# Performance work log

Hardware: AMD Instinct MI355X
Metric: run time of the kernel (lower is better)

The kernel has to match this reference:

```python
import jax, jax.numpy as jnp
import numpy as np

B, T, D, H, d = 2, 2048, 1024, 16, 64
INNER = H * d
SCALE = d ** -0.5


def _rope(x, inv_freq):
    # x: [B, H, T, d], interleaved rotary as in the torch module
    t = x.shape[2]
    pos = jnp.arange(t, dtype=jnp.float32)
    freqs = pos[:, None] * inv_freq[None, :]          # [T, d/2]
    cos_f, sin_f = jnp.cos(freqs), jnp.sin(freqs)
    x1, x2 = x[..., 0::2], x[..., 1::2]
    y1 = x1 * cos_f - x2 * sin_f
    y2 = x1 * sin_f + x2 * cos_f
    return jnp.stack([y1, y2], axis=-1).reshape(x.shape)


def setup_inputs() -> dict:
    key = jax.random.key(0)
    ks = jax.random.split(key, 6)
    x = jax.random.normal(ks[0], (B, T, D), jnp.float32)
    W_qkv = jax.random.normal(ks[1], (D, 3 * INNER), jnp.float32) * (D ** -0.5)
    W_out = jax.random.normal(ks[2], (INNER, D), jnp.float32) * (INNER ** -0.5)
    W_dt = jax.random.normal(ks[3], (D, H), jnp.float32) * 0.01
    b_dt = jnp.full((H,), -4.0, jnp.float32)
    W_gsp = jax.random.normal(ks[4], (D, INNER), jnp.float32) * 0.01
    b_gsp = jnp.full((INNER,), -3.0, jnp.float32)
    inv_freq = 1.0 / (10000.0 ** (jnp.arange(0, d, 2, dtype=jnp.float32) / d))
    return {"x": x, "W_qkv": W_qkv, "W_out": W_out, "W_dt": W_dt,
            "b_dt": b_dt, "W_gsp": W_gsp, "b_gsp": b_gsp, "inv_freq": inv_freq}


def reference(x, W_qkv, W_out, W_dt, b_dt, W_gsp, b_gsp, inv_freq):
    qkv = (x @ W_qkv).reshape(B, T, 3, H, d)
    Q = jnp.moveaxis(qkv[:, :, 0], 1, 2)   # [B,H,T,d]
    K = jnp.moveaxis(qkv[:, :, 1], 1, 2)
    V = jnp.moveaxis(qkv[:, :, 2], 1, 2)
    Q = _rope(Q, inv_freq)
    K = _rope(K, inv_freq)

    dt = jax.nn.softplus(x @ W_dt + b_dt)             # [B,T,H]
    gamma = jnp.moveaxis(jnp.exp(-dt), 1, 2)          # [B,H,T]

    p = jax.nn.sigmoid(x @ W_gsp + b_gsp).reshape(B, T, H, d)
    p = jnp.moveaxis(p, 1, 2)                          # [B,H,T,d]
    gamma_eff = gamma[..., None] * (1.0 - p) + p
    gamma_scalar = gamma_eff.mean(axis=-1)            # [B,H,T]
    V = V * (1.0 - p)

    log_gamma = jnp.log(jnp.clip(gamma_scalar, 1e-6, 1.0 - 1e-6))
    lgc = jnp.cumsum(log_gamma, axis=-1)              # [B,H,T]
    log_D = jnp.clip(lgc[..., :, None] - lgc[..., None, :], -20.0, 0.0)
    causal = jnp.tril(jnp.ones((T, T), jnp.float32))
    Dm = jnp.exp(log_D) * causal                      # [B,H,T,T]

    Wscore = jnp.einsum('bhtd,bhsd->bhts', Q * SCALE, K)
    A = Wscore * Dm
    Y = jnp.einsum('bhts,bhsd->bhtd', A, V)
    Y = jnp.moveaxis(Y, 1, 2).reshape(B, T, INNER)
    return Y @ W_out
```

## Files before the change

### kernel.cpp

```cpp
#include <hip/hip_runtime.h>
#include <hip/hip_bf16.h>
#include <math.h>

#define B_     2
#define T_     2048
#define D_     1024
#define H_     16
#define INNER_ 1024
#define NC_    4352
#define SCALE_ 0.125f

typedef unsigned short u16;
typedef short short8 __attribute__((ext_vector_type(8)));
typedef float f32x4 __attribute__((ext_vector_type(4)));
typedef unsigned short u16x4 __attribute__((ext_vector_type(4)));

__device__ __forceinline__ u16 f2bf(float x) {
  union { float f; unsigned u; } v; v.f = x;
  unsigned r = v.u + 0x7fffu + ((v.u >> 16) & 1u);
  return (u16)(r >> 16);
}
__device__ __forceinline__ float b2f(u16 x) {
  union { unsigned u; float f; } v; v.u = ((unsigned)x) << 16;
  return v.f;
}
__device__ __forceinline__ void gload16(const void* g, void* l) {
  __builtin_amdgcn_global_load_lds(
      (const __attribute__((address_space(1))) void*)g,
      (__attribute__((address_space(3))) void*)l, 16, 0, 0);
}

__global__ __launch_bounds__(256) void cast_bf16_kernel(
    const float* __restrict__ src, u16* __restrict__ dst, int n4) {
  int i = blockIdx.x * 256 + threadIdx.x;
  if (i >= n4) return;
  float4 v = *reinterpret_cast<const float4*>(src + (size_t)i * 4);
  u16x4 o; o.x = f2bf(v.x); o.y = f2bf(v.y); o.z = f2bf(v.z); o.w = f2bf(v.w);
  *reinterpret_cast<u16x4*>(dst + (size_t)i * 4) = o;
}

__global__ __launch_bounds__(256) void cast_transpose_kernel(
    const float* __restrict__ src, u16* __restrict__ dst, int K, int N) {
  __shared__ float tile[64][65];
  const int k0 = blockIdx.y * 64, n0 = blockIdx.x * 64;
  for (int e = threadIdx.x; e < 4096; e += 256) {
    int kk = e >> 6, nn = e & 63;
    tile[kk][nn] = src[(size_t)(k0 + kk) * N + n0 + nn];
  }
  __syncthreads();
  for (int e = threadIdx.x; e < 4096; e += 256) {
    int nn = e >> 6, kk = e & 63;
    dst[(size_t)(n0 + nn) * K + k0 + kk] = f2bf(tile[kk][nn]);
  }
}

__global__ __launch_bounds__(256) void wdt_transpose_kernel(
    const float* __restrict__ W_dt, u16* __restrict__ dst) {
  int i = blockIdx.x * 256 + threadIdx.x;
  int k = i >> 4, h = i & 15;
  dst[(size_t)h * D_ + k] = f2bf(W_dt[i]);
}

__global__ __launch_bounds__(256) void rope_tab_kernel(
    const float* __restrict__ inv_freq, float2* __restrict__ tab) {
  int i = blockIdx.x * 256 + threadIdx.x;
  int t = i >> 5, j = i & 31;
  float s, c;
  sincosf((float)t * inv_freq[j], &s, &c);
  tab[i] = make_float2(c, s);
}

#define SWZG(r) ((((r) & 3) ^ (((r) >> 2) & 1)))

__device__ __forceinline__ void stage_op(const u16* __restrict__ gbase, int kt,
                                         char* ldst, int h, int tid) {
  int r = h * 128 + (tid >> 2);
  int kg = (tid & 3) ^ SWZG(r);
  gload16(gbase + (size_t)r * D_ + kt * 32 + kg * 8,
          ldst + (h * 128 + (tid >> 6) * 16) * 64);
}
__device__ __forceinline__ short8 ldfrag(const char* tile, int row, int g4) {
  return *(const short8*)(tile + row * 64 + ((g4 ^ SWZG(row)) << 4));
}

__global__ __launch_bounds__(512, 2) void gemm_big(
    const u16* __restrict__ A, const u16* __restrict__ Bt,
    u16* __restrict__ C) {
  __shared__ char lds[4 * 32768];
  const int tid = threadIdx.x;
  const int w = tid >> 6, l = tid & 63;
  const int bid = blockIdx.x;
  const int xcd = bid & 7, j = bid >> 3;
  const int brow = xcd * 2 + (j >= 17 ? 1 : 0);
  const int bcol = (j >= 17) ? j - 17 : j;
  const int m0 = brow * 256, n0 = bcol * 256;
  const int wr = (w >> 2) * 128, wc = (w & 3) * 64;
  const int ql = l & 15, g4 = l >> 4;

  const u16* Ag = A + (size_t)m0 * D_;
  const u16* Bg = Bt + (size_t)n0 * D_;

  f32x4 acc[8][4] = {};

#pragma unroll
  for (int t = 0; t < 3; ++t) {
    char* bufA = lds + t * 32768;
    char* bufB = bufA + 16384;
    stage_op(Ag, t, bufA, 0, tid); stage_op(Ag, t, bufA, 1, tid);
    stage_op(Bg, t, bufB, 0, tid); stage_op(Bg, t, bufB, 1, tid);
  }

  const int NT = D_ / 32;
  for (int kt = 0; kt < NT; ++kt) {
    if (kt < NT - 2)       asm volatile("s_waitcnt vmcnt(8)" ::: "memory");
    else if (kt == NT - 2) asm volatile("s_waitcnt vmcnt(4)" ::: "memory");
    else                   asm volatile("s_waitcnt vmcnt(0)" ::: "memory");
    __builtin_amdgcn_sched_barrier(0);
    __builtin_amdgcn_s_barrier();
    __builtin_amdgcn_sched_barrier(0);

    char* bufA = lds + (kt & 3) * 32768;
    char* bufB = bufA + 16384;
    char* nbufA = lds + ((kt + 3) & 3) * 32768;
    char* nbufB = nbufA + 16384;
    const bool pre = (kt + 3 < NT);

    if (pre) {
      stage_op(Ag, kt + 3, nbufA, 0, tid);
      stage_op(Ag, kt + 3, nbufA, 1, tid);
    }
    short8 bf[4];
#pragma unroll
    for (int nf = 0; nf < 4; ++nf) bf[nf] = ldfrag(bufB, wc + nf * 16 + ql, g4);
    short8 af[4];
#pragma unroll
    for (int mf = 0; mf < 4; ++mf) af[mf] = ldfrag(bufA, wr + mf * 16 + ql, g4);
    __builtin_amdgcn_s_setprio(1);
#pragma unroll
    for (int mf = 0; mf < 4; ++mf)
#pragma unroll
      for (int nf = 0; nf < 4; ++nf)
        acc[mf][nf] = __builtin_amdgcn_mfma_f32_16x16x32_bf16(af[mf], bf[nf], acc[mf][nf], 0, 0, 0);
    __builtin_amdgcn_s_setprio(0);

    if (pre) {
      stage_op(Bg, kt + 3, nbufB, 0, tid);
      stage_op(Bg, kt + 3, nbufB, 1, tid);
    }
    short8 af2[4];
#pragma unroll
    for (int mf = 0; mf < 4; ++mf) af2[mf] = ldfrag(bufA, wr + 64 + mf * 16 + ql, g4);
    __builtin_amdgcn_s_setprio(1);
#pragma unroll
    for (int mf = 0; mf < 4; ++mf)
#pragma unroll
      for (int nf = 0; nf < 4; ++nf)
        acc[mf + 4][nf] = __builtin_amdgcn_mfma_f32_16x16x32_bf16(af2[mf], bf[nf], acc[mf + 4][nf], 0, 0, 0);
    __builtin_amdgcn_s_setprio(0);
  }

#pragma unroll
  for (int mf = 0; mf < 8; ++mf) {
#pragma unroll
    for (int r = 0; r < 4; ++r) {
      size_t row = (size_t)(m0 + wr + mf * 16 + g4 * 4 + r);
      size_t base = row * NC_ + n0 + wc + ql;
#pragma unroll
      for (int nf = 0; nf < 4; ++nf)
        C[base + nf * 16] = f2bf(acc[mf][nf][r]);
    }
  }
}

template <bool BF16OUT>
__global__ __launch_bounds__(256) void gemm_bt(
    const u16* __restrict__ A, const u16* __restrict__ Bt,
    void* __restrict__ Cv, int M, int N, int K) {
  __shared__ u16 As[128 * 64] __attribute__((aligned(16)));
  __shared__ u16 Bs[128 * 64] __attribute__((aligned(16)));
  const int tid = threadIdx.x;
  const int w = tid >> 6, l = tid & 63;
  const int m0 = blockIdx.y * 128, n0 = blockIdx.x * 128;
  const int wr = (w >> 1) * 64, wc = (w & 1) * 64;
  const int srow = l >> 3;
  const int kgrp = ((l & 7) ^ srow) * 8;

  f32x4 acc[4][4] = {};

  for (int kt = 0; kt < K; kt += 64) {
    if (kt) __syncthreads();
#pragma unroll
    for (int i = 0; i < 4; ++i) {
      int c = w * 4 + i;
      int row = c * 8 + srow;
      gload16(A + (size_t)(m0 + row) * K + kt + kgrp, (char*)As + c * 1024);
      gload16(Bt + (size_t)(n0 + row) * K + kt + kgrp, (char*)Bs + c * 1024);
    }
    __syncthreads();
#pragma unroll
    for (int kk = 0; kk < 2; ++kk) {
      short8 af[4], bf[4];
#pragma unroll
      for (int i = 0; i < 4; ++i) {
        int ra = wr + i * 16 + (l & 15);
        int sa = kk * 4 + (l >> 4);
        af[i] = *(const short8*)((const char*)As + ra * 128 + ((sa ^ (ra & 7)) << 4));
        int rb = wc + i * 16 + (l & 15);
        bf[i] = *(const short8*)((const char*)Bs + rb * 128 + ((sa ^ (rb & 7)) << 4));
      }
#pragma unroll
      for (int i = 0; i < 4; ++i)
#pragma unroll
        for (int j = 0; j < 4; ++j)
          acc[i][j] = __builtin_amdgcn_mfma_f32_16x16x32_bf16(af[i], bf[j], acc[i][j], 0, 0, 0);
    }
  }
#pragma unroll
  for (int i = 0; i < 4; ++i) {
#pragma unroll
    for (int r = 0; r < 4; ++r) {
      size_t row = (size_t)(m0 + wr + i * 16 + (l >> 4) * 4 + r);
      size_t base = row * N + n0 + wc + (l & 15);
#pragma unroll
      for (int j = 0; j < 4; ++j) {
        if (BF16OUT) ((u16*)Cv)[base + j * 16] = f2bf(acc[i][j][r]);
        else         ((float*)Cv)[base + j * 16] = acc[i][j][r];
      }
    }
  }
}

__global__ __launch_bounds__(256) void pointwise_kernel(
    const u16* __restrict__ C, const float* __restrict__ b_dt,
    const float* __restrict__ b_gsp, const float2* __restrict__ tab,
    u16* __restrict__ Qb, u16* __restrict__ Kb, u16* __restrict__ Vb,
    float* __restrict__ lg) {
  const int row = blockIdx.x * 4 + (threadIdx.x >> 6);
  const int l = threadIdx.x & 63;
  const int b = row >> 11, t = row & (T_ - 1);
  const int h = l >> 2;
  const int dd0 = (l & 3) * 16;
  const int col = h * 64 + dd0;
  const size_t cb = (size_t)row * NC_;

  float dtv = b2f(C[cb + 4096 + h]) + b_dt[h];
  float sp = (dtv > 20.f) ? dtv : log1pf(__expf(dtv));
  const float gh = __expf(-sp);

  const short8* qp = (const short8*)(C + cb + col);
  const short8* kp = (const short8*)(C + cb + 1024 + col);
  const short8* vp = (const short8*)(C + cb + 2048 + col);
  const short8* pp = (const short8*)(C + cb + 3072 + col);
  short8 q0 = qp[0], q1 = qp[1];
  short8 k0 = kp[0], k1 = kp[1];
  short8 v0 = vp[0], v1 = vp[1];
  short8 pr0 = pp[0], pr1 = pp[1];

  float ge = 0.f;
  short8 vo0, vo1;
#pragma unroll
  for (int i = 0; i < 8; ++i) {
    float pv = b2f((u16)pr0[i]) + b_gsp[col + i];
    float p = 1.f / (1.f + __expf(-pv));
    ge += gh * (1.f - p) + p;
    vo0[i] = (short)f2bf(b2f((u16)v0[i]) * (1.f - p));
    float pv1 = b2f((u16)pr1[i]) + b_gsp[col + 8 + i];
    float p1 = 1.f / (1.f + __expf(-pv1));
    ge += gh * (1.f - p1) + p1;
    vo1[i] = (short)f2bf(b2f((u16)v1[i]) * (1.f - p1));
  }
  const size_t hm = (((size_t)(b * H_ + h)) * T_ + t) * 64 + dd0;
  ((short8*)(Vb + hm))[0] = vo0;
  ((short8*)(Vb + hm))[1] = vo1;

  ge += __shfl_xor(ge, 1);
  ge += __shfl_xor(ge, 2);
  if ((l & 3) == 0) {
    float gs = ge * (1.f / 64.f);
    gs = fminf(fmaxf(gs, 1e-6f), 1.f - 1e-6f);
    lg[((size_t)(b * H_ + h)) * T_ + t] = logf(gs);
  }

  short8 qo0, qo1, ko0, ko1;
  const float2* cs = tab + t * 32 + (dd0 >> 1);
#pragma unroll
  for (int m = 0; m < 4; ++m) {
    float2 c0 = cs[m];
    float qa = b2f((u16)q0[2 * m]), qb = b2f((u16)q0[2 * m + 1]);
    qo0[2 * m]     = (short)f2bf((qa * c0.x - qb * c0.y) * SCALE_);
    qo0[2 * m + 1] = (short)f2bf((qa * c0.y + qb * c0.x) * SCALE_);
    float ka = b2f((u16)k0[2 * m]), kb = b2f((u16)k0[2 * m + 1]);
    ko0[2 * m]     = (short)f2bf(ka * c0.x - kb * c0.y);
    ko0[2 * m + 1] = (short)f2bf(ka * c0.y + kb * c0.x);
    float2 c1 = cs[4 + m];
    float qa1 = b2f((u16)q1[2 * m]), qb1 = b2f((u16)q1[2 * m + 1]);
    qo1[2 * m]     = (short)f2bf((qa1 * c1.x - qb1 * c1.y) * SCALE_);
    qo1[2 * m + 1] = (short)f2bf((qa1 * c1.y + qb1 * c1.x) * SCALE_);
    float ka1 = b2f((u16)k1[2 * m]), kb1 = b2f((u16)k1[2 * m + 1]);
    ko1[2 * m]     = (short)f2bf(ka1 * c1.x - kb1 * c1.y);
    ko1[2 * m + 1] = (short)f2bf(ka1 * c1.y + kb1 * c1.x);
  }
  ((short8*)(Qb + hm))[0] = qo0; ((short8*)(Qb + hm))[1] = qo1;
  ((short8*)(Kb + hm))[0] = ko0; ((short8*)(Kb + hm))[1] = ko1;
}

__global__ __launch_bounds__(256) void scan_kernel(
    const float* __restrict__ lg, float* __restrict__ lgc) {
  const size_t base = (size_t)blockIdx.x * T_;
  const int tid = threadIdx.x;
  __shared__ float sums[256];
  float loc[8];
  float run = 0.f;
#pragma unroll
  for (int i = 0; i < 8; ++i) { run += lg[base + tid * 8 + i]; loc[i] = run; }
  sums[tid] = run;
  __syncthreads();
  if (tid == 0) {
    float r = 0.f;
    for (int i = 0; i < 256; ++i) { float v = sums[i]; sums[i] = r; r += v; }
  }
  __syncthreads();
  const float off = sums[tid];
#pragma unroll
  for (int i = 0; i < 8; ++i) lgc[base + tid * 8 + i] = off + loc[i];
}

__global__ __launch_bounds__(256) void kv_prep_kernel(
    const u16* __restrict__ Kb, const u16* __restrict__ Vb,
    const float* __restrict__ lgc, u16* __restrict__ Kp,
    u16* __restrict__ Vtg) {
  const int stile = blockIdx.x;
  const int bh = blockIdx.y;
  const int tid = threadIdx.x;
  __shared__ u16 vt[64][72];
  const size_t base = ((size_t)bh * T_ + (size_t)stile * 64) * 64;
  const float* lgp = lgc + (size_t)bh * T_;
  const float lgb = lgp[stile * 64];
#pragma unroll
  for (int i = 0; i < 2; ++i) {
    int c = tid * 2 + i;
    int row = c >> 3, k8 = (c & 7) * 8;
    float beta = __expf(lgb - lgp[stile * 64 + row]);
    short8 kv = *(const short8*)(Kb + base + row * 64 + k8);
    short8 ko;
#pragma unroll
    for (int j = 0; j < 8; ++j) ko[j] = (short)f2bf(b2f((u16)kv[j]) * beta);
    *(short8*)(Kp + base + row * 64 + k8) = ko;
    short8 vv = *(const short8*)(Vb + base + row * 64 + k8);
#pragma unroll
    for (int j = 0; j < 8; ++j) vt[row][k8 + j] = (u16)vv[j];
  }
  __syncthreads();
#pragma unroll
  for (int i = 0; i < 2; ++i) {
    int c = tid * 2 + i;
    int dd = c >> 3, t8 = (c & 7) * 8;
    short8 o;
#pragma unroll
    for (int j = 0; j < 8; ++j) o[j] = (short)vt[t8 + j][dd];
    *(short8*)(Vtg + ((size_t)bh * 64 + dd) * T_ + stile * 64 + t8) = o;
  }
}

__global__ __launch_bounds__(256) void attn_mfma(
    const u16* __restrict__ Qb, const u16* __restrict__ Kp,
    const u16* __restrict__ Vtg, const float* __restrict__ lgc,
    u16* __restrict__ Y) {
  const int i = blockIdx.x;
  const int tt = (i >> 3) & 31;
  const int bh = (i & 7) + ((i >> 8) << 3);
  const int b = bh >> 4, h = bh & 15;
  const int tid = threadIdx.x, w = tid >> 6, l = tid & 63;
  __shared__ u16 Qs[64 * 64] __attribute__((aligned(16)));
  __shared__ u16 Ks[64 * 64] __attribute__((aligned(16)));
  __shared__ u16 Vs[64 * 64] __attribute__((aligned(16)));
  const u16* Qg = Qb + (size_t)bh * T_ * 64;
  const u16* Kg = Kp + (size_t)bh * T_ * 64;
  const u16* Vg = Vtg + (size_t)bh * 64 * T_;
  const float* lgp = lgc + (size_t)bh * T_;

  const int srow = l >> 3;
  const int kgrp = ((l & 7) ^ srow) * 8;
  const int ql = l & 15, g4 = l >> 4;

#pragma unroll
  for (int i2 = 0; i2 < 2; ++i2) {
    int c = w * 2 + i2;
    int row = c * 8 + srow;
    gload16(Qg + (size_t)(tt * 64 + row) * 64 + kgrp, (char*)Qs + c * 1024);
  }
  const float lgq = lgp[tt * 64 + w * 16 + ql];
  const float lgtop = lgp[tt * 64];
  __syncthreads();

  short8 qf[2];
#pragma unroll
  for (int kk = 0; kk < 2; ++kk) {
    int row = w * 16 + ql;
    int slot = kk * 4 + g4;
    qf[kk] = *(const short8*)((const char*)Qs + row * 128 + ((slot ^ (row & 7)) << 4));
  }
  char* Pw = (char*)Qs + w * 2048;
  const int pswz = (ql & 7) << 4;

  f32x4 yacc[4] = {};

  for (int st = tt; st >= 0; --st) {
    if (st < tt && lgtop - lgp[st * 64 + 63] <= -20.f) break;
    __syncthreads();
#pragma unroll
    for (int i2 = 0; i2 < 2; ++i2) {
      int c = w * 2 + i2;
      int row = c * 8 + srow;
      gload16(Kg + (size_t)(st * 64 + row) * 64 + kgrp, (char*)Ks + c * 1024);
      gload16(Vg + (size_t)row * T_ + st * 64 + kgrp, (char*)Vs + c * 1024);
    }
    const float alpha = __expf(lgq - lgp[st * 64]);
    __syncthreads();

    const bool diag = (st == tt);
#pragma unroll
    for (int n = 0; n < 4; ++n) {
      f32x4 s = {};
#pragma unroll
      for (int kk = 0; kk < 2; ++kk) {
        int row = n * 16 + ql;
        int slot = kk * 4 + g4;
        short8 kf = *(const short8*)((const char*)Ks + row * 128 + ((slot ^ (row & 7)) << 4));
        s = __builtin_amdgcn_mfma_f32_16x16x32_bf16(kf, qf[kk], s, 0, 0, 0);
      }
      u16x4 pk;
#pragma unroll
      for (int r = 0; r < 4; ++r) {
        float pv = s[r] * alpha;
        if (diag && (n * 16 + g4 * 4 + r) > (w * 16 + ql)) pv = 0.f;
        pk[r] = f2bf(pv);
      }
      *(u16x4*)(Pw + ((ql * 128 + n * 32 + g4 * 8) ^ pswz)) = pk;
    }
#pragma unroll
    for (int kk = 0; kk < 2; ++kk) {
      short8 pf = *(const short8*)(Pw + ((ql * 128 + kk * 64 + g4 * 16) ^ pswz));
#pragma unroll
      for (int n2 = 0; n2 < 4; ++n2) {
        int row = n2 * 16 + ql;
        int slot = kk * 4 + g4;
        short8 vf = *(const short8*)((const char*)Vs + row * 128 + ((slot ^ (row & 7)) << 4));
        yacc[n2] = __builtin_amdgcn_mfma_f32_16x16x32_bf16(pf, vf, yacc[n2], 0, 0, 0);
      }
    }
  }

#pragma unroll
  for (int n2 = 0; n2 < 4; ++n2)
#pragma unroll
    for (int r = 0; r < 4; ++r) {
      size_t row = (size_t)(b * T_) + tt * 64 + w * 16 + g4 * 4 + r;
      Y[row * INNER_ + h * 64 + n2 * 16 + ql] = f2bf(yacc[n2][r]);
    }
}

extern "C" void kernel_launch(void* const* d_in, const int* in_sizes, int n_in,
                              void* d_out, int out_size, void* d_ws, size_t ws_size,
                              hipStream_t stream) {
  const float* x        = (const float*)d_in[0];
  const float* W_qkv    = (const float*)d_in[1];
  const float* W_out    = (const float*)d_in[2];
  const float* W_dt     = (const float*)d_in[3];
  const float* b_dt     = (const float*)d_in[4];
  const float* W_gsp    = (const float*)d_in[5];
  const float* b_gsp    = (const float*)d_in[6];
  const float* inv_freq = (const float*)d_in[7];
  float* out = (float*)d_out;

  const int M = B_ * T_;
  char* p = (char*)d_ws;
  auto alloc = [&](size_t bytes) {
    char* r = p; p += (bytes + 255) & ~(size_t)255; return r;
  };
  u16*    xb    = (u16*)alloc((size_t)M * D_ * 2);
  u16*    Wcombt= (u16*)alloc((size_t)NC_ * D_ * 2);
  u16*    Woutt = (u16*)alloc((size_t)D_ * INNER_ * 2);
  u16*    Cqkvp = (u16*)alloc((size_t)M * NC_ * 2);
  u16*    Qb    = (u16*)alloc((size_t)B_ * H_ * T_ * 64 * 2);
  u16*    Kb    = (u16*)alloc((size_t)B_ * H_ * T_ * 64 * 2);
  u16*    Vb    = (u16*)alloc((size_t)B_ * H_ * T_ * 64 * 2);
  float*  lg    = (float*)alloc((size_t)B_ * H_ * T_ * 4);
  float*  lgc   = (float*)alloc((size_t)B_ * H_ * T_ * 4);
  float2* tab   = (float2*)alloc((size_t)T_ * 32 * 8);
  u16*    Kp    = Cqkvp;
  u16*    Vtg   = Cqkvp + (size_t)4 * 1024 * 1024;
  u16*    Yb    = Cqkvp + (size_t)8 * 1024 * 1024;

  cast_bf16_kernel<<<(M * D_ / 4 + 255) / 256, 256, 0, stream>>>(x, xb, M * D_ / 4);
  rope_tab_kernel<<<T_ * 32 / 256, 256, 0, stream>>>(inv_freq, tab);
  cast_transpose_kernel<<<dim3(3 * INNER_ / 64, D_ / 64), 256, 0, stream>>>(
      W_qkv, Wcombt, D_, 3 * INNER_);
  cast_transpose_kernel<<<dim3(INNER_ / 64, D_ / 64), 256, 0, stream>>>(
      W_gsp, Wcombt + (size_t)3 * INNER_ * D_, D_, INNER_);
  wdt_transpose_kernel<<<64, 256, 0, stream>>>(W_dt, Wcombt + (size_t)4096 * D_);
  cast_transpose_kernel<<<dim3(D_ / 64, INNER_ / 64), 256, 0, stream>>>(
      W_out, Woutt, INNER_, D_);

  gemm_big<<<272, 512, 0, stream>>>(xb, Wcombt, Cqkvp);

  pointwise_kernel<<<M / 4, 256, 0, stream>>>(Cqkvp, b_dt, b_gsp, tab,
                                              Qb, Kb, Vb, lg);
  scan_kernel<<<B_ * H_, 256, 0, stream>>>(lg, lgc);
  kv_prep_kernel<<<dim3(T_ / 64, B_ * H_), 256, 0, stream>>>(Kb, Vb, lgc, Kp, Vtg);

  attn_mfma<<<1024, 256, 0, stream>>>(Qb, Kp, Vtg, lgc, Yb);

  gemm_bt<false><<<dim3(D_ / 128, M / 128), 256, 0, stream>>>(
      Yb, Woutt, out, M, D_, INNER_);
}
```

Before: 170.0 us.

## Fuse prep kernels, split gamma projection, double-buffer attention and output GEMM

Merges the cast, transpose, W_dt and rope-table kernels into one prep launch. Moves the dt projection out of the big GEMM into a small dot-product kernel, so the QKV GEMM drops from 4352 to 4096 columns and runs on an even 256-block grid. Double-buffers the K/V tiles in the attention loop and the A/B tiles in the output GEMM so global loads overlap MFMA work, and adds XCD-aware block mapping. The decay scaling now goes onto V instead of K, which removes one pass over K in kv_prep but changes where bf16 rounding happens.

```diff
diff --git a/kernel.cpp b/kernel.cpp
--- a/kernel.cpp
+++ b/kernel.cpp
@@ -7,7 +7,7 @@
 #define D_     1024
 #define H_     16
 #define INNER_ 1024
-#define NC_    4352
+#define NC_    4096
 #define SCALE_ 0.125f
 
 typedef unsigned short u16;
@@ -30,44 +30,74 @@
       (__attribute__((address_space(3))) void*)l, 16, 0, 0);
 }
 
-__global__ __launch_bounds__(256) void cast_bf16_kernel(
-    const float* __restrict__ src, u16* __restrict__ dst, int n4) {
-  int i = blockIdx.x * 256 + threadIdx.x;
-  if (i >= n4) return;
-  float4 v = *reinterpret_cast<const float4*>(src + (size_t)i * 4);
-  u16x4 o; o.x = f2bf(v.x); o.y = f2bf(v.y); o.z = f2bf(v.z); o.w = f2bf(v.w);
-  *reinterpret_cast<u16x4*>(dst + (size_t)i * 4) = o;
-}
-
-__global__ __launch_bounds__(256) void cast_transpose_kernel(
-    const float* __restrict__ src, u16* __restrict__ dst, int K, int N) {
-  __shared__ float tile[64][65];
-  const int k0 = blockIdx.y * 64, n0 = blockIdx.x * 64;
-  for (int e = threadIdx.x; e < 4096; e += 256) {
-    int kk = e >> 6, nn = e & 63;
-    tile[kk][nn] = src[(size_t)(k0 + kk) * N + n0 + nn];
-  }
-  __syncthreads();
-  for (int e = threadIdx.x; e < 4096; e += 256) {
-    int nn = e >> 6, kk = e & 63;
-    dst[(size_t)(n0 + nn) * K + k0 + kk] = f2bf(tile[kk][nn]);
-  }
-}
-
-__global__ __launch_bounds__(256) void wdt_transpose_kernel(
-    const float* __restrict__ W_dt, u16* __restrict__ dst) {
-  int i = blockIdx.x * 256 + threadIdx.x;
-  int k = i >> 4, h = i & 15;
-  dst[(size_t)h * D_ + k] = f2bf(W_dt[i]);
-}
-
-__global__ __launch_bounds__(256) void rope_tab_kernel(
-    const float* __restrict__ inv_freq, float2* __restrict__ tab) {
-  int i = blockIdx.x * 256 + threadIdx.x;
-  int t = i >> 5, j = i & 31;
-  float s, c;
-  sincosf((float)t * inv_freq[j], &s, &c);
-  tab[i] = make_float2(c, s);
+__global__ __launch_bounds__(256) void prep_kernel(
+    const float* __restrict__ x, const float* __restrict__ W_qkv,
+    const float* __restrict__ W_gsp, const float* __restrict__ W_out,
+    const float* __restrict__ W_dt, const float* __restrict__ inv_freq,
+    u16* __restrict__ xb, u16* __restrict__ Wcombt, u16* __restrict__ Woutt,
+    u16* __restrict__ Wdtb, float2* __restrict__ tab) {
+  const int bid = blockIdx.x, tid = threadIdx.x;
+  if (bid < 1280) {
+    const float* src; u16* dst; int N, nx, ky;
+    if (bid < 768)       { src = W_qkv; dst = Wcombt;                N = 3072; nx = bid % 48;          ky = bid / 48; }
+    else if (bid < 1024) { src = W_gsp; dst = Wcombt + 3072 * 1024;  N = 1024; nx = (bid - 768) % 16;  ky = (bid - 768) / 16; }
+    else                 { src = W_out; dst = Woutt;                 N = 1024; nx = (bid - 1024) % 16; ky = (bid - 1024) / 16; }
+    __shared__ float tile[64][65];
+    const int k0 = ky * 64, n0 = nx * 64;
+    for (int e = tid; e < 4096; e += 256) {
+      int kk = e >> 6, nn = e & 63;
+      tile[kk][nn] = src[(size_t)(k0 + kk) * N + n0 + nn];
+    }
+    __syncthreads();
+    for (int e = tid; e < 4096; e += 256) {
+      int nn = e >> 6, kk = e & 63;
+      dst[(size_t)(n0 + nn) * 1024 + k0 + kk] = f2bf(tile[kk][nn]);
+    }
+  } else if (bid < 1344) {
+    int i = (bid - 1280) * 256 + tid;
+    int k = i >> 4, h = i & 15;
+    Wdtb[(size_t)h * D_ + k] = f2bf(W_dt[i]);
+  } else if (bid < 1600) {
+    int i = (bid - 1344) * 256 + tid;
+    int t = i >> 5, j = i & 31;
+    float s, c;
+    sincosf((float)t * inv_freq[j], &s, &c);
+    tab[i] = make_float2(c, s);
+  } else {
+    int base = (bid - 1600) * 1024 + tid;
+#pragma unroll
+    for (int r = 0; r < 4; ++r) {
+      int i = base + r * 256;
+      float4 v = *reinterpret_cast<const float4*>(x + (size_t)i * 4);
+      u16x4 o; o.x = f2bf(v.x); o.y = f2bf(v.y); o.z = f2bf(v.z); o.w = f2bf(v.w);
+      *reinterpret_cast<u16x4*>(xb + (size_t)i * 4) = o;
+    }
+  }
+}
+
+__global__ __launch_bounds__(256) void gamma_kernel(
+    const u16* __restrict__ xb, const u16* __restrict__ Wdtb,
+    const float* __restrict__ b_dt, float* __restrict__ gam) {
+  const int row = blockIdx.x * 4 + (threadIdx.x >> 6);
+  const int l = threadIdx.x & 63;
+  const int h = l >> 2;
+  const int kc = (l & 3) * 256;
+  const short8* xp = (const short8*)(xb + (size_t)row * D_ + kc);
+  const short8* wp = (const short8*)(Wdtb + h * D_ + kc);
+  float s = 0.f;
+#pragma unroll
+  for (int i = 0; i < 32; ++i) {
+    short8 xv = xp[i], wv = wp[i];
+#pragma unroll
+    for (int j = 0; j < 8; ++j) s += b2f((u16)xv[j]) * b2f((u16)wv[j]);
+  }
+  s += __shfl_xor(s, 1);
+  s += __shfl_xor(s, 2);
+  if ((l & 3) == 0) {
+    float v = s + b_dt[h];
+    float sp = (v > 20.f) ? v : log1pf(__expf(v));
+    gam[row * H_ + h] = __expf(-sp);
+  }
 }
 
 #define SWZG(r) ((((r) & 3) ^ (((r) >> 2) & 1)))
@@ -90,9 +120,9 @@
   const int tid = threadIdx.x;
   const int w = tid >> 6, l = tid & 63;
   const int bid = blockIdx.x;
-  const int xcd = bid & 7, j = bid >> 3;
-  const int brow = xcd * 2 + (j >= 17 ? 1 : 0);
-  const int bcol = (j >= 17) ? j - 17 : j;
+  const int xcd = bid & 7, idx = bid >> 3;
+  const int brow = (xcd >> 1) * 4 + (idx & 3);
+  const int bcol = (xcd & 1) * 8 + (idx >> 2);
   const int m0 = brow * 256, n0 = bcol * 256;
   const int wr = (w >> 2) * 128, wc = (w & 3) * 64;
   const int ql = l & 15, g4 = l >> 4;
@@ -176,27 +206,45 @@
 __global__ __launch_bounds__(256) void gemm_bt(
     const u16* __restrict__ A, const u16* __restrict__ Bt,
     void* __restrict__ Cv, int M, int N, int K) {
-  __shared__ u16 As[128 * 64] __attribute__((aligned(16)));
-  __shared__ u16 Bs[128 * 64] __attribute__((aligned(16)));
-  const int tid = threadIdx.x;
-  const int w = tid >> 6, l = tid & 63;
-  const int m0 = blockIdx.y * 128, n0 = blockIdx.x * 128;
+  __shared__ u16 As[2][128 * 64] __attribute__((aligned(16)));
+  __shared__ u16 Bs[2][128 * 64] __attribute__((aligned(16)));
+  const int tid = threadIdx.x, w = tid >> 6, l = tid & 63;
+  const int rpx = (M >> 7) >> 3;
+  const int bid = blockIdx.x;
+  const int xcd = bid & 7, idx = bid >> 3;
+  const int brow = xcd * rpx + (idx % rpx);
+  const int bcol = idx / rpx;
+  const int m0 = brow * 128, n0 = bcol * 128;
   const int wr = (w >> 1) * 64, wc = (w & 1) * 64;
   const int srow = l >> 3;
   const int kgrp = ((l & 7) ^ srow) * 8;
 
   f32x4 acc[4][4] = {};
 
-  for (int kt = 0; kt < K; kt += 64) {
-    if (kt) __syncthreads();
+  auto stage = [&](int kt, int bs) {
 #pragma unroll
     for (int i = 0; i < 4; ++i) {
       int c = w * 4 + i;
       int row = c * 8 + srow;
-      gload16(A + (size_t)(m0 + row) * K + kt + kgrp, (char*)As + c * 1024);
-      gload16(Bt + (size_t)(n0 + row) * K + kt + kgrp, (char*)Bs + c * 1024);
-    }
-    __syncthreads();
+      gload16(A + (size_t)(m0 + row) * K + kt * 64 + kgrp, (char*)As[bs] + c * 1024);
+      gload16(Bt + (size_t)(n0 + row) * K + kt * 64 + kgrp, (char*)Bs[bs] + c * 1024);
+    }
+  };
+
+  stage(0, 0);
+  const int NT = K >> 6;
+  for (int kt = 0; kt < NT; ++kt) {
+    if (kt + 1 < NT) {
+      stage(kt + 1, (kt + 1) & 1);
+      asm volatile("s_waitcnt vmcnt(8)" ::: "memory");
+    } else {
+      asm volatile("s_waitcnt vmcnt(0)" ::: "memory");
+    }
+    __builtin_amdgcn_sched_barrier(0);
+    __builtin_amdgcn_s_barrier();
+    __builtin_amdgcn_sched_barrier(0);
+    const char* Asb = (const char*)As[kt & 1];
+    const char* Bsb = (const char*)Bs[kt & 1];
 #pragma unroll
     for (int kk = 0; kk < 2; ++kk) {
       short8 af[4], bf[4];
@@ -204,9 +252,9 @@
       for (int i = 0; i < 4; ++i) {
         int ra = wr + i * 16 + (l & 15);
         int sa = kk * 4 + (l >> 4);
-        af[i] = *(const short8*)((const char*)As + ra * 128 + ((sa ^ (ra & 7)) << 4));
+        af[i] = *(const short8*)(Asb + ra * 128 + ((sa ^ (ra & 7)) << 4));
         int rb = wc + i * 16 + (l & 15);
-        bf[i] = *(const short8*)((const char*)Bs + rb * 128 + ((sa ^ (rb & 7)) << 4));
+        bf[i] = *(const short8*)(Bsb + rb * 128 + ((sa ^ (rb & 7)) << 4));
       }
 #pragma unroll
       for (int i = 0; i < 4; ++i)
@@ -214,6 +262,7 @@
         for (int j = 0; j < 4; ++j)
           acc[i][j] = __builtin_amdgcn_mfma_f32_16x16x32_bf16(af[i], bf[j], acc[i][j], 0, 0, 0);
     }
+    if (kt + 1 < NT) __builtin_amdgcn_s_barrier();
   }
 #pragma unroll
   for (int i = 0; i < 4; ++i) {
@@ -231,7 +280,7 @@
 }
 
 __global__ __launch_bounds__(256) void pointwise_kernel(
-    const u16* __restrict__ C, const float* __restrict__ b_dt,
+    const u16* __restrict__ C, const float* __restrict__ gam,
     const float* __restrict__ b_gsp, const float2* __restrict__ tab,
     u16* __restrict__ Qb, u16* __restrict__ Kb, u16* __restrict__ Vb,
     float* __restrict__ lg) {
@@ -243,10 +292,7 @@
   const int col = h * 64 + dd0;
   const size_t cb = (size_t)row * NC_;
 
-  float dtv = b2f(C[cb + 4096 + h]) + b_dt[h];
-  float sp = (dtv > 20.f) ? dtv : log1pf(__expf(dtv));
-  const float gh = __expf(-sp);
-
+  const float gh = gam[row * H_ + h];
   const short8* qp = (const short8*)(C + cb + col);
   const short8* kp = (const short8*)(C + cb + 1024 + col);
   const short8* vp = (const short8*)(C + cb + 2048 + col);
@@ -326,8 +372,7 @@
 }
 
 __global__ __launch_bounds__(256) void kv_prep_kernel(
-    const u16* __restrict__ Kb, const u16* __restrict__ Vb,
-    const float* __restrict__ lgc, u16* __restrict__ Kp,
+    const u16* __restrict__ Vb, const float* __restrict__ lgc,
     u16* __restrict__ Vtg) {
   const int stile = blockIdx.x;
   const int bh = blockIdx.y;
@@ -341,14 +386,9 @@
     int c = tid * 2 + i;
     int row = c >> 3, k8 = (c & 7) * 8;
     float beta = __expf(lgb - lgp[stile * 64 + row]);
-    short8 kv = *(const short8*)(Kb + base + row * 64 + k8);
-    short8 ko;
-#pragma unroll
-    for (int j = 0; j < 8; ++j) ko[j] = (short)f2bf(b2f((u16)kv[j]) * beta);
-    *(short8*)(Kp + base + row * 64 + k8) = ko;
     short8 vv = *(const short8*)(Vb + base + row * 64 + k8);
 #pragma unroll
-    for (int j = 0; j < 8; ++j) vt[row][k8 + j] = (u16)vv[j];
+    for (int j = 0; j < 8; ++j) vt[row][k8 + j] = f2bf(b2f((u16)vv[j]) * beta);
   }
   __syncthreads();
 #pragma unroll
@@ -363,7 +403,7 @@
 }
 
 __global__ __launch_bounds__(256) void attn_mfma(
-    const u16* __restrict__ Qb, const u16* __restrict__ Kp,
+    const u16* __restrict__ Qb, const u16* __restrict__ Kb,
     const u16* __restrict__ Vtg, const float* __restrict__ lgc,
     u16* __restrict__ Y) {
   const int i = blockIdx.x;
@@ -372,10 +412,10 @@
   const int b = bh >> 4, h = bh & 15;
   const int tid = threadIdx.x, w = tid >> 6, l = tid & 63;
   __shared__ u16 Qs[64 * 64] __attribute__((aligned(16)));
-  __shared__ u16 Ks[64 * 64] __attribute__((aligned(16)));
-  __shared__ u16 Vs[64 * 64] __attribute__((aligned(16)));
+  __shared__ u16 Ks[2][64 * 64] __attribute__((aligned(16)));
+  __shared__ u16 Vs[2][64 * 64] __attribute__((aligned(16)));
   const u16* Qg = Qb + (size_t)bh * T_ * 64;
-  const u16* Kg = Kp + (size_t)bh * T_ * 64;
+  const u16* Kg = Kb + (size_t)bh * T_ * 64;
   const u16* Vg = Vtg + (size_t)bh * 64 * T_;
   const float* lgp = lgc + (size_t)bh * T_;
 
@@ -405,20 +445,38 @@
 
   f32x4 yacc[4] = {};
 
-  for (int st = tt; st >= 0; --st) {
-    if (st < tt && lgtop - lgp[st * 64 + 63] <= -20.f) break;
-    __syncthreads();
+  {
+    const int bs = tt & 1;
 #pragma unroll
     for (int i2 = 0; i2 < 2; ++i2) {
-      int c = w * 2 + i2;
-      int row = c * 8 + srow;
-      gload16(Kg + (size_t)(st * 64 + row) * 64 + kgrp, (char*)Ks + c * 1024);
-      gload16(Vg + (size_t)row * T_ + st * 64 + kgrp, (char*)Vs + c * 1024);
-    }
+      int c = w * 2 + i2, row = c * 8 + srow;
+      gload16(Kg + (size_t)(tt * 64 + row) * 64 + kgrp, (char*)Ks[bs] + c * 1024);
+      gload16(Vg + (size_t)row * T_ + tt * 64 + kgrp, (char*)Vs[bs] + c * 1024);
+    }
+  }
+
+  for (int st = tt;; --st) {
+    const int bs = st & 1;
+    const bool last = (st == 0) || (lgtop - lgp[(st - 1) * 64 + 63] <= -20.f);
+    if (!last) {
+#pragma unroll
+      for (int i2 = 0; i2 < 2; ++i2) {
+        int c = w * 2 + i2, row = c * 8 + srow;
+        gload16(Kg + (size_t)((st - 1) * 64 + row) * 64 + kgrp, (char*)Ks[bs ^ 1] + c * 1024);
+        gload16(Vg + (size_t)row * T_ + (st - 1) * 64 + kgrp, (char*)Vs[bs ^ 1] + c * 1024);
+      }
+      asm volatile("s_waitcnt vmcnt(4)" ::: "memory");
+    } else {
+      asm volatile("s_waitcnt vmcnt(0)" ::: "memory");
+    }
+    __builtin_amdgcn_sched_barrier(0);
+    __builtin_amdgcn_s_barrier();
+    __builtin_amdgcn_sched_barrier(0);
+
     const float alpha = __expf(lgq - lgp[st * 64]);
-    __syncthreads();
-
     const bool diag = (st == tt);
+    const char* Ksb = (const char*)Ks[bs];
+    const char* Vsb = (const char*)Vs[bs];
 #pragma unroll
     for (int n = 0; n < 4; ++n) {
       f32x4 s = {};
@@ -426,7 +484,7 @@
       for (int kk = 0; kk < 2; ++kk) {
         int row = n * 16 + ql;
         int slot = kk * 4 + g4;
-        short8 kf = *(const short8*)((const char*)Ks + row * 128 + ((slot ^ (row & 7)) << 4));
+        short8 kf = *(const short8*)(Ksb + row * 128 + ((slot ^ (row & 7)) << 4));
         s = __builtin_amdgcn_mfma_f32_16x16x32_bf16(kf, qf[kk], s, 0, 0, 0);
       }
       u16x4 pk;
@@ -445,10 +503,12 @@
       for (int n2 = 0; n2 < 4; ++n2) {
         int row = n2 * 16 + ql;
         int slot = kk * 4 + g4;
-        short8 vf = *(const short8*)((const char*)Vs + row * 128 + ((slot ^ (row & 7)) << 4));
+        short8 vf = *(const short8*)(Vsb + row * 128 + ((slot ^ (row & 7)) << 4));
         yacc[n2] = __builtin_amdgcn_mfma_f32_16x16x32_bf16(pf, vf, yacc[n2], 0, 0, 0);
       }
     }
+    if (last) break;
+    __builtin_amdgcn_s_barrier();
   }
 
 #pragma unroll
@@ -481,36 +541,29 @@
   u16*    xb    = (u16*)alloc((size_t)M * D_ * 2);
   u16*    Wcombt= (u16*)alloc((size_t)NC_ * D_ * 2);
   u16*    Woutt = (u16*)alloc((size_t)D_ * INNER_ * 2);
+  u16*    Wdtb  = (u16*)alloc((size_t)H_ * D_ * 2);
   u16*    Cqkvp = (u16*)alloc((size_t)M * NC_ * 2);
   u16*    Qb    = (u16*)alloc((size_t)B_ * H_ * T_ * 64 * 2);
   u16*    Kb    = (u16*)alloc((size_t)B_ * H_ * T_ * 64 * 2);
   u16*    Vb    = (u16*)alloc((size_t)B_ * H_ * T_ * 64 * 2);
+  float*  gam   = (float*)alloc((size_t)M * H_ * 4);
   float*  lg    = (float*)alloc((size_t)B_ * H_ * T_ * 4);
   float*  lgc   = (float*)alloc((size_t)B_ * H_ * T_ * 4);
   float2* tab   = (float2*)alloc((size_t)T_ * 32 * 8);
-  u16*    Kp    = Cqkvp;
-  u16*    Vtg   = Cqkvp + (size_t)4 * 1024 * 1024;
-  u16*    Yb    = Cqkvp + (size_t)8 * 1024 * 1024;
-
-  cast_bf16_kernel<<<(M * D_ / 4 + 255) / 256, 256, 0, stream>>>(x, xb, M * D_ / 4);
-  rope_tab_kernel<<<T_ * 32 / 256, 256, 0, stream>>>(inv_freq, tab);
-  cast_transpose_kernel<<<dim3(3 * INNER_ / 64, D_ / 64), 256, 0, stream>>>(
-      W_qkv, Wcombt, D_, 3 * INNER_);
-  cast_transpose_kernel<<<dim3(INNER_ / 64, D_ / 64), 256, 0, stream>>>(
-      W_gsp, Wcombt + (size_t)3 * INNER_ * D_, D_, INNER_);
-  wdt_transpose_kernel<<<64, 256, 0, stream>>>(W_dt, Wcombt + (size_t)4096 * D_);
-  cast_transpose_kernel<<<dim3(D_ / 64, INNER_ / 64), 256, 0, stream>>>(
-      W_out, Woutt, INNER_, D_);
-
-  gemm_big<<<272, 512, 0, stream>>>(xb, Wcombt, Cqkvp);
-
-  pointwise_kernel<<<M / 4, 256, 0, stream>>>(Cqkvp, b_dt, b_gsp, tab,
+  u16*    Vtg   = Cqkvp;
+  u16*    Yb    = Cqkvp + (size_t)4 * 1024 * 1024;
+
+  prep_kernel<<<2624, 256, 0, stream>>>(x, W_qkv, W_gsp, W_out, W_dt, inv_freq,
+                                        xb, Wcombt, Woutt, Wdtb, tab);
+  gamma_kernel<<<M / 4, 256, 0, stream>>>(xb, Wdtb, b_dt, gam);
+  gemm_big<<<256, 512, 0, stream>>>(xb, Wcombt, Cqkvp);
+
+  pointwise_kernel<<<M / 4, 256, 0, stream>>>(Cqkvp, gam, b_gsp, tab,
                                               Qb, Kb, Vb, lg);
   scan_kernel<<<B_ * H_, 256, 0, stream>>>(lg, lgc);
-  kv_prep_kernel<<<dim3(T_ / 64, B_ * H_), 256, 0, stream>>>(Kb, Vb, lgc, Kp, Vtg);
-
-  attn_mfma<<<1024, 256, 0, stream>>>(Qb, Kp, Vtg, lgc, Yb);
-
-  gemm_bt<false><<<dim3(D_ / 128, M / 128), 256, 0, stream>>>(
-      Yb, Woutt, out, M, D_, INNER_);
-}
+  kv_prep_kernel<<<dim3(T_ / 64, B_ * H_), 256, 0, stream>>>(Vb, lgc, Vtg);
+
+  attn_mfma<<<1024, 256, 0, stream>>>(Qb, Kb, Vtg, lgc, Yb);
+
+  gemm_bt<false><<<256, 256, 0, stream>>>(Yb, Woutt, out, M, D_, INNER_);
+}
```

Result: faster. 156.2 us (-8.1%).
